# Kernel tuning notes

Measured on AMD Instinct MI355X. Metric: run time of the kernel, lower is better.

## Reference

```python
import jax, jax.numpy as jnp
import numpy as np

B, S, HID = 2, 2048, 2048
H, HKV = 16, 4
D = HID // H          # 128
N_REP = H // HKV      # 4
ROPE_THETA = 1000000.0


def _rope_tables(seq_len, head_dim, theta):
    inv_freq = 1.0 / (theta ** (jnp.arange(0, head_dim, 2, dtype=jnp.float32) / head_dim))
    freqs = jnp.arange(seq_len, dtype=jnp.float32)[:, None] * inv_freq[None, :]  # [S, D/2]
    emb = jnp.concatenate([freqs, freqs], axis=-1)  # [S, D]
    return jnp.cos(emb), jnp.sin(emb)


def setup_inputs() -> dict:
    key = jax.random.key(0)
    ks = jax.random.split(key, 6)
    cos, sin = _rope_tables(S, D, ROPE_THETA)
    sc = 0.02
    return {
        "x": jax.random.normal(ks[0], (B, S, HID), jnp.float32),
        "cos": cos,
        "sin": sin,
        "Wq": jax.random.normal(ks[1], (HID, H * D), jnp.float32) * sc,
        "Wk": jax.random.normal(ks[2], (HID, HKV * D), jnp.float32) * sc,
        "Wv": jax.random.normal(ks[3], (HID, HKV * D), jnp.float32) * sc,
        "Wo": jax.random.normal(ks[4], (H * D, HID), jnp.float32) * sc,
    }


def _rotate_half(t):
    t1, t2 = jnp.split(t, 2, axis=-1)
    return jnp.concatenate([-t2, t1], axis=-1)


def reference(x, cos, sin, Wq, Wk, Wv, Wo):
    b, s, _ = x.shape
    q = (x @ Wq).reshape(b, s, H, D)    # [b,s,H,d]
    k = (x @ Wk).reshape(b, s, HKV, D)  # [b,s,Hkv,d]
    v = (x @ Wv).reshape(b, s, HKV, D)

    # RoPE (cos/sin broadcast over head axis)
    c = cos[:s, None, :]  # [s,1,d]
    sn = sin[:s, None, :]
    q = q * c + _rotate_half(q) * sn
    k = k * c + _rotate_half(k) * sn

    # GQA: repeat kv heads (interleaved, matching repeat_kv)
    k = jnp.repeat(k, N_REP, axis=2)  # [b,s,H,d]
    v = jnp.repeat(v, N_REP, axis=2)

    q = q.transpose(0, 2, 1, 3)  # [b,H,s,d]
    k = k.transpose(0, 2, 1, 3)
    v = v.transpose(0, 2, 1, 3)

    scale = 1.0 / jnp.sqrt(jnp.asarray(D, x.dtype))
    scores = jnp.einsum("bhqd,bhkd->bhqk", q, k) * scale
    causal = jnp.tril(jnp.ones((s, s), dtype=bool))
    scores = jnp.where(causal[None, None], scores, jnp.asarray(-jnp.inf, scores.dtype))
    probs = jax.nn.softmax(scores, axis=-1)
    out = jnp.einsum("bhqk,bhkd->bhqd", probs, v)
    out = out.transpose(0, 2, 1, 3).reshape(b, s, H * D)
    return out @ Wo
```

## Files before the change

kernel.cpp:

```cpp
#include <hip/hip_runtime.h>
#include <cstdint>

#define B_    2
#define S_    2048
#define HID_  2048
#define H_    16
#define HKV_  4
#define D_    128
#define SCALE_ 0.08838834764831845f
#define LOG2E_ 1.4426950408889634f
#define K1_   (SCALE_ * LOG2E_)
#define THRS_ 62.75f

typedef __bf16 bf16x8 __attribute__((ext_vector_type(8)));
typedef float  f32x4  __attribute__((ext_vector_type(4)));
using u16 = unsigned short;

static __device__ __forceinline__ u16 f2bf(float f) {
  union { float f; uint32_t u; } c; c.f = f;
  uint32_t u = c.u;
  return (u16)((u + 0x7FFFu + ((u >> 16) & 1u)) >> 16);
}
static __device__ __forceinline__ float bf2f(u16 h) {
  union { uint32_t u; float f; } c; c.u = ((uint32_t)h) << 16;
  return c.f;
}
static __device__ __forceinline__ void async16(const u16* g, u16* lds) {
  __builtin_amdgcn_global_load_lds((const __attribute__((address_space(1))) void*)g,
                                   (__attribute__((address_space(3))) void*)lds, 16, 0, 0);
}

__global__ __launch_bounds__(256) void prep_cast_weights(const float* __restrict__ x,
                                                         const float* __restrict__ Wq,
                                                         const float* __restrict__ Wk,
                                                         const float* __restrict__ Wv,
                                                         const float* __restrict__ Wo,
                                                         u16* __restrict__ xb,
                                                         u16* __restrict__ Wt,
                                                         u16* __restrict__ Wot) {
  __shared__ float tile[32][33];
  const int t = blockIdx.x;
  const int tid = threadIdx.x;
  if (t < 8192) {
    const int i = t * 256 + tid;
    float4 v = ((const float4*)x)[i];
    ushort4 o;
    o.x = f2bf(v.x); o.y = f2bf(v.y); o.z = f2bf(v.z); o.w = f2bf(v.w);
    ((ushort4*)xb)[i] = o;
    return;
  }
  const int tw = t - 8192;
  const float* W; u16* Dst; int N, lt;
  if (tw < 4096)      { W = Wq; Dst = Wt;                        N = 2048; lt = tw; }
  else if (tw < 5120) { W = Wk; Dst = Wt + (size_t)2048 * 2048;  N = 512;  lt = tw - 4096; }
  else if (tw < 6144) { W = Wv; Dst = Wt + (size_t)2560 * 2048;  N = 512;  lt = tw - 5120; }
  else                { W = Wo; Dst = Wot;                       N = 2048; lt = tw - 6144; }
  const int tx = tid & 31, ty = tid >> 5;
  const int tn = N >> 5;
  const int n0 = (lt % tn) * 32, k0 = (lt / tn) * 32;
#pragma unroll
  for (int j = 0; j < 32; j += 8)
    tile[ty + j][tx] = W[(size_t)(k0 + ty + j) * N + n0 + tx];
  __syncthreads();
#pragma unroll
  for (int j = 0; j < 32; j += 8)
    Dst[(size_t)(n0 + ty + j) * 2048 + k0 + tx] = f2bf(tile[tx][ty + j]);
}

__global__ __launch_bounds__(256) void prep_rope_vt(const u16* __restrict__ qkv,
                                                    const float* __restrict__ cosb,
                                                    const float* __restrict__ sinb,
                                                    u16* __restrict__ Qr, u16* __restrict__ Kr,
                                                    u16* __restrict__ Vt) {
  __shared__ u16 tile[32][34];
  const int NQ2 = B_ * S_ * H_ * 32;
  const int NK2 = B_ * S_ * HKV_ * 32;
  const int blk = blockIdx.x;
  const int tid = threadIdx.x;
  if (blk < 10240) {
    const int idx = blk * 256 + tid;
    if (idx < NQ2) {
      const int j = (idx & 31) * 2, rest = idx >> 5;
      const int h = rest & 15, srow = rest >> 4;
      const int s = srow & (S_ - 1);
      const u16* base = qkv + (size_t)srow * 3072 + h * 128;
      const float2 cc = *(const float2*)&cosb[s * 128 + j];
      const float2 ss = *(const float2*)&sinb[s * 128 + j];
      const ushort2 av = *(const ushort2*)&base[j];
      const ushort2 bv = *(const ushort2*)&base[j + 64];
      const float a0 = bf2f(av.x), a1 = bf2f(av.y);
      const float b0 = bf2f(bv.x), b1 = bf2f(bv.y);
      const size_t qo = (((size_t)(srow >> 11) * H_ + h) * S_ + s) * D_;
      ushort2 lo, hi;
      lo.x = f2bf(a0 * cc.x - b0 * ss.x); lo.y = f2bf(a1 * cc.y - b1 * ss.y);
      hi.x = f2bf(b0 * cc.x + a0 * ss.x); hi.y = f2bf(b1 * cc.y + a1 * ss.y);
      *(ushort2*)&Qr[qo + j]      = lo;
      *(ushort2*)&Qr[qo + j + 64] = hi;
    } else if (idx < NQ2 + NK2) {
      const int t2 = idx - NQ2;
      const int j = (t2 & 31) * 2, rest = t2 >> 5;
      const int kv = rest & 3, srow = rest >> 2;
      const int s = srow & (S_ - 1);
      const u16* base = qkv + (size_t)srow * 3072 + 2048 + kv * 128;
      const float2 cc = *(const float2*)&cosb[s * 128 + j];
      const float2 ss = *(const float2*)&sinb[s * 128 + j];
      const ushort2 av = *(const ushort2*)&base[j];
      const ushort2 bv = *(const ushort2*)&base[j + 64];
      const float a0 = bf2f(av.x), a1 = bf2f(av.y);
      const float b0 = bf2f(bv.x), b1 = bf2f(bv.y);
      const size_t ko = (((size_t)(srow >> 11) * HKV_ + kv) * S_ + s) * D_;
      ushort2 lo, hi;
      lo.x = f2bf(a0 * cc.x - b0 * ss.x); lo.y = f2bf(a1 * cc.y - b1 * ss.y);
      hi.x = f2bf(b0 * cc.x + a0 * ss.x); hi.y = f2bf(b1 * cc.y + a1 * ss.y);
      *(ushort2*)&Kr[ko + j]      = lo;
      *(ushort2*)&Kr[ko + j + 64] = hi;
    }
    return;
  }
  const int lt = blk - 10240;
  const int bx = lt & 3, by = (lt >> 2) & 63, mat = lt >> 8;
  const int b = mat >> 2, kv = mat & 3;
  const int d0 = bx * 32, s0 = by * 32;
  const int tx = tid & 31, ty = tid >> 5;
#pragma unroll
  for (int j = 0; j < 32; j += 8)
    tile[ty + j][tx] = qkv[(size_t)(b * S_ + s0 + ty + j) * 3072 + 2560 + kv * 128 + d0 + tx];
  __syncthreads();
  const int sc  = s0 + tx;
  const int t64 = sc & 63;
  const int p   = ((t64 >> 5) * 4 + ((t64 >> 2) & 3)) * 8 + ((t64 >> 4) & 1) * 4 + (t64 & 3);
  const int scp = (sc & ~63) | p;
#pragma unroll
  for (int j = 0; j < 32; j += 8)
    Vt[((size_t)mat * D_ + d0 + ty + j) * S_ + scp] = tile[tx][ty + j];
}

template<int BF16OUT>
__global__ __launch_bounds__(256, 4) void gemm_bt(const u16* __restrict__ A,
                                                  const u16* __restrict__ Bt,
                                                  void* __restrict__ Cv,
                                                  int M, int N, int K, int gx) {
  const int nwg = (int)gridDim.x;
  const int bid = (int)blockIdx.x;
  const int qq = nwg >> 3, rr = nwg & 7;
  const int xcd = bid & 7, pos = bid >> 3;
  const int wg = ((xcd < rr) ? xcd * (qq + 1) : rr * (qq + 1) + (xcd - rr) * qq) + pos;
  const int bm = (wg % gx) * 128;
  const int bn = (wg / gx) * 128;

  __shared__ __align__(16) u16 Ash[128 * 64];
  __shared__ __align__(16) u16 Bsh[128 * 64];
  const int tid = threadIdx.x;
  const int w = tid >> 6, l = tid & 63;
  const int wm = (w >> 1) * 64, wn = (w & 1) * 64;

  const f32x4 z4 = {0.f, 0.f, 0.f, 0.f};
  f32x4 acc[4][4];
#pragma unroll
  for (int i = 0; i < 4; ++i)
#pragma unroll
    for (int j = 0; j < 4; ++j) acc[i][j] = z4;

  const int srow = w * 8 + (l >> 3);
  const int schunk = l & 7;

  for (int k0 = 0; k0 < K; k0 += 64) {
#pragma unroll
    for (int i = 0; i < 4; ++i) {
      const int row = i * 32 + srow;
      const int ch = schunk ^ (row & 7);
      async16(A + (size_t)(bm + row) * K + k0 + ch * 8, &Ash[(i * 4 + w) * 512]);
      async16(Bt + (size_t)(bn + row) * K + k0 + ch * 8, &Bsh[(i * 4 + w) * 512]);
    }
    asm volatile("s_waitcnt vmcnt(0)" ::: "memory");
    __syncthreads();
#pragma unroll
    for (int kc = 0; kc < 2; ++kc) {
      bf16x8 af[4], bfr[4];
#pragma unroll
      for (int mi = 0; mi < 4; ++mi) {
        const int r = wm + mi * 16 + (l & 15);
        const int c2 = (kc * 4 + (l >> 4)) ^ (r & 7);
        af[mi] = *(const bf16x8*)&Ash[r * 64 + c2 * 8];
      }
#pragma unroll
      for (int ni = 0; ni < 4; ++ni) {
        const int r = wn + ni * 16 + (l & 15);
        const int c2 = (kc * 4 + (l >> 4)) ^ (r & 7);
        bfr[ni] = *(const bf16x8*)&Bsh[r * 64 + c2 * 8];
      }
#pragma unroll
      for (int mi = 0; mi < 4; ++mi)
#pragma unroll
        for (int ni = 0; ni < 4; ++ni)
          acc[mi][ni] = __builtin_amdgcn_mfma_f32_16x16x32_bf16(af[mi], bfr[ni], acc[mi][ni], 0, 0, 0);
    }
    __syncthreads();
  }
#pragma unroll
  for (int mi = 0; mi < 4; ++mi) {
    const int r0 = bm + wm + mi * 16 + ((l >> 4) << 2);
#pragma unroll
    for (int ni = 0; ni < 4; ++ni) {
      const int c = bn + wn + ni * 16 + (l & 15);
#pragma unroll
      for (int j = 0; j < 4; ++j) {
        if (BF16OUT) ((u16*)Cv)[(size_t)(r0 + j) * N + c] = f2bf(acc[mi][ni][j]);
        else         ((float*)Cv)[(size_t)(r0 + j) * N + c] = acc[mi][ni][j];
      }
    }
  }
}

__global__ __launch_bounds__(256, 3) void attn_kernel(const u16* __restrict__ Q,
                                                      const u16* __restrict__ Kc,
                                                      const u16* __restrict__ Vt,
                                                      u16* __restrict__ O) {
  const int bid = blockIdx.x;
  const int p   = bid & 7;
  const int hs  = (bid >> 3) & 3;
  const int qt  = 31 - (bid >> 5);
  const int b   = p >> 2;
  const int kvh = p & 3;
  const int h   = kvh * 4 + hs;
  const int bh  = b * 16 + h;
  const int tid = threadIdx.x;
  const int w = tid >> 6, l = tid & 63;
  const int g = l >> 4, c = l & 15;
  const int q0 = qt * 64;

  __shared__ __align__(16) u16 Ksh[64 * 128];
  __shared__ __align__(16) u16 VshF[2 * 128 * 64];

  const u16* Kbase = Kc + ((size_t)(b * HKV_ + kvh) * S_) * D_;
  const u16* Vbase = Vt + ((size_t)(b * HKV_ + kvh) * D_) * S_;

  bf16x8 qf[4];
  {
    const u16* qp = Q + ((size_t)bh * S_ + q0 + w * 16 + c) * D_ + g * 8;
#pragma unroll
    for (int kc = 0; kc < 4; ++kc) qf[kc] = *(const bf16x8*)(qp + kc * 32);
  }

  int srcK[4], srcV[4];
#pragma unroll
  for (int i = 0; i < 4; ++i) {
    const int rK = i * 16 + w * 4 + g;
    srcK[i] = rK * 128 + (c ^ (rK & 7)) * 8;
    const int dV = i * 32 + w * 8 + (l >> 3);
    srcV[i] = dV * S_ + ((l & 7) ^ (dV & 7)) * 8;
  }

  const f32x4 z4 = {0.f, 0.f, 0.f, 0.f};
  f32x4 oacc[8];
#pragma unroll
  for (int nb = 0; nb < 8; ++nb) oacc[nb] = z4;
  float m_i = -1e30f, l_i = 0.f;

  auto stageK = [&](int kv0) {
#pragma unroll
    for (int i = 0; i < 4; ++i)
      async16(Kbase + (size_t)kv0 * 128 + srcK[i], &Ksh[i * 2048 + w * 512]);
  };
  auto stageV = [&](int buf, int kv0) {
#pragma unroll
    for (int i = 0; i < 4; ++i)
      async16(Vbase + kv0 + srcV[i], &VshF[buf * 8192 + i * 2048 + w * 512]);
  };

  const int nt = qt + 1;
  stageV(0, 0);
  stageK(0);

  for (int t = 0; t < nt; ++t) {
    const int cur = t & 1;
    asm volatile("s_waitcnt vmcnt(0)" ::: "memory");
    __syncthreads();
    if (t + 1 < nt) stageV(cur ^ 1, (t + 1) << 6);

    f32x4 sf[4];
#pragma unroll
    for (int nb = 0; nb < 4; ++nb) sf[nb] = z4;

    __builtin_amdgcn_s_setprio(1);
#pragma unroll
    for (int kc = 0; kc < 4; ++kc) {
#pragma unroll
      for (int nb = 0; nb < 4; ++nb) {
        const int r = nb * 16 + c;
        const int s2 = (kc * 4 + g) ^ (c & 7);
        const bf16x8 kf = *(const bf16x8*)&Ksh[r * 128 + s2 * 8];
        sf[nb] = __builtin_amdgcn_mfma_f32_16x16x32_bf16(kf, qf[kc], sf[nb], 0, 0, 0);
      }
    }
    __builtin_amdgcn_s_setprio(0);

    __syncthreads();
    if (t + 1 < nt) stageK((t + 1) << 6);

    {
      const int kv0 = t << 6;
      const int qcol = q0 + w * 16 + c;
      const bool doMask = (t == nt - 1);
      float mx = -3e38f;
#pragma unroll
      for (int nb = 0; nb < 4; ++nb)
#pragma unroll
        for (int jj = 0; jj < 4; ++jj) {
          float sv = sf[nb][jj];
          if (doMask) {
            const int kk = kv0 + nb * 16 + g * 4 + jj;
            sv = (kk > qcol) ? -3e38f : sv;
            sf[nb][jj] = sv;
          }
          mx = fmaxf(mx, sv);
        }
      mx = fmaxf(mx, __shfl_xor(mx, 16));
      mx = fmaxf(mx, __shfl_xor(mx, 32));

      if (__all(mx <= m_i + THRS_)) {
        const float mk = m_i * K1_;
        float rs = 0.f;
#pragma unroll
        for (int nb = 0; nb < 4; ++nb)
#pragma unroll
          for (int jj = 0; jj < 4; ++jj) {
            const float p2 = exp2f(fmaf(sf[nb][jj], K1_, -mk));
            sf[nb][jj] = p2;
            rs += p2;
          }
        rs += __shfl_xor(rs, 16);
        rs += __shfl_xor(rs, 32);
        l_i += rs;
      } else {
        const float mnew = fmaxf(m_i, mx);
        const float fsc = exp2f((m_i - mnew) * K1_);
        m_i = mnew;
        const float mk = mnew * K1_;
        float rs = 0.f;
#pragma unroll
        for (int nb = 0; nb < 4; ++nb)
#pragma unroll
          for (int jj = 0; jj < 4; ++jj) {
            const float p2 = exp2f(fmaf(sf[nb][jj], K1_, -mk));
            sf[nb][jj] = p2;
            rs += p2;
          }
        rs += __shfl_xor(rs, 16);
        rs += __shfl_xor(rs, 32);
        l_i = l_i * fsc + rs;
        float fq[4];
#pragma unroll
        for (int j = 0; j < 4; ++j) fq[j] = __shfl(fsc, g * 4 + j);
#pragma unroll
        for (int nb = 0; nb < 8; ++nb)
#pragma unroll
          for (int j = 0; j < 4; ++j) oacc[nb][j] *= fq[j];
      }
    }

    bf16x8 pa, pb;
#pragma unroll
    for (int jj = 0; jj < 4; ++jj) {
      pa[jj] = (__bf16)sf[0][jj]; pa[4 + jj] = (__bf16)sf[1][jj];
      pb[jj] = (__bf16)sf[2][jj]; pb[4 + jj] = (__bf16)sf[3][jj];
    }

    const char* Vb = (const char*)&VshF[cur * 8192] + c * 128;
    __builtin_amdgcn_s_setprio(1);
#pragma unroll
    for (int kc2 = 0; kc2 < 2; ++kc2) {
      const bf16x8 pfr = kc2 ? pb : pa;
      const int s2v = ((kc2 * 4 + g) ^ (c & 7)) << 4;
#pragma unroll
      for (int nb = 0; nb < 8; ++nb) {
        const bf16x8 vf = *(const bf16x8*)(Vb + nb * 2048 + s2v);
        oacc[nb] = __builtin_amdgcn_mfma_f32_16x16x32_bf16(pfr, vf, oacc[nb], 0, 0, 0);
      }
    }
    __builtin_amdgcn_s_setprio(0);
  }

#pragma unroll
  for (int j = 0; j < 4; ++j) {
    const float li = __shfl(l_i, g * 4 + j);
    const float inv = 1.f / li;
    const int srow = q0 + w * 16 + g * 4 + j;
    u16* op = O + ((size_t)(b * S_ + srow)) * HID_ + h * D_ + c;
#pragma unroll
    for (int nb = 0; nb < 8; ++nb) op[nb * 16] = f2bf(oacc[nb][j] * inv);
  }
}

extern "C" void kernel_launch(void* const* d_in, const int* in_sizes, int n_in,
                              void* d_out, int out_size, void* d_ws, size_t ws_size,
                              hipStream_t stream) {
  const float* x    = (const float*)d_in[0];
  const float* cosb = (const float*)d_in[1];
  const float* sinb = (const float*)d_in[2];
  const float* Wq   = (const float*)d_in[3];
  const float* Wk   = (const float*)d_in[4];
  const float* Wv   = (const float*)d_in[5];
  const float* Wo   = (const float*)d_in[6];
  float* out = (float*)d_out;

  u16*   xb   = (u16*)d_ws;
  u16*   Wt   = xb  + (size_t)4096 * 2048;
  u16*   Wot  = Wt  + (size_t)3072 * 2048;
  u16*   qkv  = Wot + (size_t)2048 * 2048;
  u16*   Qr   = qkv + (size_t)4096 * 3072;
  u16*   Kr   = Qr  + (size_t)B_ * H_ * S_ * D_;
  u16*   Vtb  = Kr  + (size_t)B_ * HKV_ * S_ * D_;
  u16*   Ob   = Vtb + (size_t)B_ * HKV_ * S_ * D_;

  prep_cast_weights<<<dim3(18432), 256, 0, stream>>>(x, Wq, Wk, Wv, Wo, xb, Wt, Wot);

  gemm_bt<1><<<dim3(768), 256, 0, stream>>>(xb, Wt, qkv, 4096, 3072, 2048, 32);

  prep_rope_vt<<<dim3(12288), 256, 0, stream>>>(qkv, cosb, sinb, Qr, Kr, Vtb);

  attn_kernel<<<dim3(1024), 256, 0, stream>>>(Qr, Kr, Vtb, Ob);

  gemm_bt<0><<<dim3(512), 256, 0, stream>>>(Ob, Wot, out, 4096, 2048, 2048, 32);
}
```

Measured before the change: 198.6 us.

## Widen attention query tile to 128 rows with double-buffered K/V

Each attention block now covers 128 query rows, with two 16-row groups per wave, instead of 64, so every K/V tile loaded into shared memory feeds twice as many MFMAs. K is now double-buffered together with V, which removes the second barrier in each iteration. Waves skip KV tiles that lie entirely above their causal rows. The block-to-tile order changes so heavy and light query tiles are interleaved, and the launch bounds drop to 2 blocks per CU to allow more registers. In exchange the grid is halved to 512 blocks, which lowers occupancy and parallelism, and waves in a block become unevenly loaded on the diagonal tiles.

```diff
diff --git a/kernel.cpp b/kernel.cpp
--- a/kernel.cpp
+++ b/kernel.cpp
@@ -212,14 +212,14 @@
   }
 }
 
-__global__ __launch_bounds__(256, 3) void attn_kernel(const u16* __restrict__ Q,
+__global__ __launch_bounds__(256, 2) void attn_kernel(const u16* __restrict__ Q,
                                                       const u16* __restrict__ Kc,
                                                       const u16* __restrict__ Vt,
                                                       u16* __restrict__ O) {
   const int bid = blockIdx.x;
   const int p   = bid & 7;
   const int hs  = (bid >> 3) & 3;
-  const int qt  = 31 - (bid >> 5);
+  const int qt  = (bid < 256) ? (15 - (bid >> 5)) : ((bid >> 5) - 8);
   const int b   = p >> 2;
   const int kvh = p & 3;
   const int h   = kvh * 4 + hs;
@@ -227,19 +227,20 @@
   const int tid = threadIdx.x;
   const int w = tid >> 6, l = tid & 63;
   const int g = l >> 4, c = l & 15;
-  const int q0 = qt * 64;
-
-  __shared__ __align__(16) u16 Ksh[64 * 128];
+  const int q0 = qt * 128;
+
+  __shared__ __align__(16) u16 KshF[2 * 64 * 128];
   __shared__ __align__(16) u16 VshF[2 * 128 * 64];
 
   const u16* Kbase = Kc + ((size_t)(b * HKV_ + kvh) * S_) * D_;
   const u16* Vbase = Vt + ((size_t)(b * HKV_ + kvh) * D_) * S_;
 
-  bf16x8 qf[4];
-  {
-    const u16* qp = Q + ((size_t)bh * S_ + q0 + w * 16 + c) * D_ + g * 8;
-#pragma unroll
-    for (int kc = 0; kc < 4; ++kc) qf[kc] = *(const bf16x8*)(qp + kc * 32);
+  bf16x8 qf[2][4];
+#pragma unroll
+  for (int qg = 0; qg < 2; ++qg) {
+    const u16* qp = Q + ((size_t)bh * S_ + q0 + w * 32 + qg * 16 + c) * D_ + g * 8;
+#pragma unroll
+    for (int kc = 0; kc < 4; ++kc) qf[qg][kc] = *(const bf16x8*)(qp + kc * 32);
   }
 
   int srcK[4], srcV[4];
@@ -252,144 +253,153 @@
   }
 
   const f32x4 z4 = {0.f, 0.f, 0.f, 0.f};
-  f32x4 oacc[8];
-#pragma unroll
-  for (int nb = 0; nb < 8; ++nb) oacc[nb] = z4;
-  float m_i = -1e30f, l_i = 0.f;
-
-  auto stageK = [&](int kv0) {
-#pragma unroll
-    for (int i = 0; i < 4; ++i)
-      async16(Kbase + (size_t)kv0 * 128 + srcK[i], &Ksh[i * 2048 + w * 512]);
+  f32x4 oacc[2][8];
+#pragma unroll
+  for (int qg = 0; qg < 2; ++qg)
+#pragma unroll
+    for (int nb = 0; nb < 8; ++nb) oacc[qg][nb] = z4;
+  float m_i[2] = {-1e30f, -1e30f}, l_i[2] = {0.f, 0.f};
+
+  auto stage = [&](int buf, int kv0) {
+#pragma unroll
+    for (int i = 0; i < 4; ++i) {
+      async16(Kbase + (size_t)kv0 * 128 + srcK[i], &KshF[buf * 8192 + i * 2048 + w * 512]);
+      async16(Vbase + kv0 + srcV[i],               &VshF[buf * 8192 + i * 2048 + w * 512]);
+    }
   };
-  auto stageV = [&](int buf, int kv0) {
-#pragma unroll
-    for (int i = 0; i < 4; ++i)
-      async16(Vbase + kv0 + srcV[i], &VshF[buf * 8192 + i * 2048 + w * 512]);
-  };
-
-  const int nt = qt + 1;
-  stageV(0, 0);
-  stageK(0);
+
+  const int nt = 2 * (qt + 1);
+  stage(0, 0);
 
   for (int t = 0; t < nt; ++t) {
     const int cur = t & 1;
+    const int kv0 = t << 6;
     asm volatile("s_waitcnt vmcnt(0)" ::: "memory");
     __syncthreads();
-    if (t + 1 < nt) stageV(cur ^ 1, (t + 1) << 6);
-
-    f32x4 sf[4];
-#pragma unroll
-    for (int nb = 0; nb < 4; ++nb) sf[nb] = z4;
-
-    __builtin_amdgcn_s_setprio(1);
-#pragma unroll
-    for (int kc = 0; kc < 4; ++kc) {
-#pragma unroll
-      for (int nb = 0; nb < 4; ++nb) {
-        const int r = nb * 16 + c;
-        const int s2 = (kc * 4 + g) ^ (c & 7);
-        const bf16x8 kf = *(const bf16x8*)&Ksh[r * 128 + s2 * 8];
-        sf[nb] = __builtin_amdgcn_mfma_f32_16x16x32_bf16(kf, qf[kc], sf[nb], 0, 0, 0);
-      }
-    }
-    __builtin_amdgcn_s_setprio(0);
-
-    __syncthreads();
-    if (t + 1 < nt) stageK((t + 1) << 6);
-
-    {
-      const int kv0 = t << 6;
-      const int qcol = q0 + w * 16 + c;
-      const bool doMask = (t == nt - 1);
-      float mx = -3e38f;
-#pragma unroll
-      for (int nb = 0; nb < 4; ++nb)
-#pragma unroll
-        for (int jj = 0; jj < 4; ++jj) {
-          float sv = sf[nb][jj];
-          if (doMask) {
-            const int kk = kv0 + nb * 16 + g * 4 + jj;
-            sv = (kk > qcol) ? -3e38f : sv;
-            sf[nb][jj] = sv;
+    if (t + 1 < nt) stage(cur ^ 1, (t + 1) << 6);
+
+    if (kv0 <= q0 + w * 32 + 31) {
+      const u16* Kb = &KshF[cur * 8192];
+
+      f32x4 sf[2][4];
+#pragma unroll
+      for (int qg = 0; qg < 2; ++qg)
+#pragma unroll
+        for (int nb = 0; nb < 4; ++nb) sf[qg][nb] = z4;
+
+      __builtin_amdgcn_s_setprio(1);
+#pragma unroll
+      for (int kc = 0; kc < 4; ++kc) {
+#pragma unroll
+        for (int nb = 0; nb < 4; ++nb) {
+          const int r = nb * 16 + c;
+          const int s2 = (kc * 4 + g) ^ (c & 7);
+          const bf16x8 kf = *(const bf16x8*)&Kb[r * 128 + s2 * 8];
+          sf[0][nb] = __builtin_amdgcn_mfma_f32_16x16x32_bf16(kf, qf[0][kc], sf[0][nb], 0, 0, 0);
+          sf[1][nb] = __builtin_amdgcn_mfma_f32_16x16x32_bf16(kf, qf[1][kc], sf[1][nb], 0, 0, 0);
+        }
+      }
+      __builtin_amdgcn_s_setprio(0);
+
+#pragma unroll
+      for (int qg = 0; qg < 2; ++qg) {
+        const int qcol = q0 + w * 32 + qg * 16 + c;
+        const bool doMask = (kv0 + 63 > q0 + w * 32 + qg * 16);
+        float mx = -3e38f;
+#pragma unroll
+        for (int nb = 0; nb < 4; ++nb)
+#pragma unroll
+          for (int jj = 0; jj < 4; ++jj) {
+            float sv = sf[qg][nb][jj];
+            if (doMask) {
+              const int kk = kv0 + nb * 16 + g * 4 + jj;
+              sv = (kk > qcol) ? -3e38f : sv;
+              sf[qg][nb][jj] = sv;
+            }
+            mx = fmaxf(mx, sv);
           }
-          mx = fmaxf(mx, sv);
+        mx = fmaxf(mx, __shfl_xor(mx, 16));
+        mx = fmaxf(mx, __shfl_xor(mx, 32));
+
+        if (__all(mx <= m_i[qg] + THRS_)) {
+          const float mk = m_i[qg] * K1_;
+          float rs = 0.f;
+#pragma unroll
+          for (int nb = 0; nb < 4; ++nb)
+#pragma unroll
+            for (int jj = 0; jj < 4; ++jj) {
+              const float p2 = exp2f(fmaf(sf[qg][nb][jj], K1_, -mk));
+              sf[qg][nb][jj] = p2;
+              rs += p2;
+            }
+          rs += __shfl_xor(rs, 16);
+          rs += __shfl_xor(rs, 32);
+          l_i[qg] += rs;
+        } else {
+          const float mnew = fmaxf(m_i[qg], mx);
+          const float fsc = exp2f((m_i[qg] - mnew) * K1_);
+          m_i[qg] = mnew;
+          const float mk = mnew * K1_;
+          float rs = 0.f;
+#pragma unroll
+          for (int nb = 0; nb < 4; ++nb)
+#pragma unroll
+            for (int jj = 0; jj < 4; ++jj) {
+              const float p2 = exp2f(fmaf(sf[qg][nb][jj], K1_, -mk));
+              sf[qg][nb][jj] = p2;
+              rs += p2;
+            }
+          rs += __shfl_xor(rs, 16);
+          rs += __shfl_xor(rs, 32);
+          l_i[qg] = l_i[qg] * fsc + rs;
+          float fq[4];
+#pragma unroll
+          for (int j = 0; j < 4; ++j) fq[j] = __shfl(fsc, g * 4 + j);
+#pragma unroll
+          for (int nb = 0; nb < 8; ++nb)
+#pragma unroll
+            for (int j = 0; j < 4; ++j) oacc[qg][nb][j] *= fq[j];
         }
-      mx = fmaxf(mx, __shfl_xor(mx, 16));
-      mx = fmaxf(mx, __shfl_xor(mx, 32));
-
-      if (__all(mx <= m_i + THRS_)) {
-        const float mk = m_i * K1_;
-        float rs = 0.f;
-#pragma unroll
-        for (int nb = 0; nb < 4; ++nb)
-#pragma unroll
-          for (int jj = 0; jj < 4; ++jj) {
-            const float p2 = exp2f(fmaf(sf[nb][jj], K1_, -mk));
-            sf[nb][jj] = p2;
-            rs += p2;
-          }
-        rs += __shfl_xor(rs, 16);
-        rs += __shfl_xor(rs, 32);
-        l_i += rs;
-      } else {
-        const float mnew = fmaxf(m_i, mx);
-        const float fsc = exp2f((m_i - mnew) * K1_);
-        m_i = mnew;
-        const float mk = mnew * K1_;
-        float rs = 0.f;
-#pragma unroll
-        for (int nb = 0; nb < 4; ++nb)
-#pragma unroll
-          for (int jj = 0; jj < 4; ++jj) {
-            const float p2 = exp2f(fmaf(sf[nb][jj], K1_, -mk));
-            sf[nb][jj] = p2;
-            rs += p2;
-          }
-        rs += __shfl_xor(rs, 16);
-        rs += __shfl_xor(rs, 32);
-        l_i = l_i * fsc + rs;
-        float fq[4];
-#pragma unroll
-        for (int j = 0; j < 4; ++j) fq[j] = __shfl(fsc, g * 4 + j);
-#pragma unroll
-        for (int nb = 0; nb < 8; ++nb)
-#pragma unroll
-          for (int j = 0; j < 4; ++j) oacc[nb][j] *= fq[j];
-      }
-    }
-
-    bf16x8 pa, pb;
-#pragma unroll
-    for (int jj = 0; jj < 4; ++jj) {
-      pa[jj] = (__bf16)sf[0][jj]; pa[4 + jj] = (__bf16)sf[1][jj];
-      pb[jj] = (__bf16)sf[2][jj]; pb[4 + jj] = (__bf16)sf[3][jj];
-    }
-
-    const char* Vb = (const char*)&VshF[cur * 8192] + c * 128;
-    __builtin_amdgcn_s_setprio(1);
-#pragma unroll
-    for (int kc2 = 0; kc2 < 2; ++kc2) {
-      const bf16x8 pfr = kc2 ? pb : pa;
-      const int s2v = ((kc2 * 4 + g) ^ (c & 7)) << 4;
-#pragma unroll
-      for (int nb = 0; nb < 8; ++nb) {
-        const bf16x8 vf = *(const bf16x8*)(Vb + nb * 2048 + s2v);
-        oacc[nb] = __builtin_amdgcn_mfma_f32_16x16x32_bf16(pfr, vf, oacc[nb], 0, 0, 0);
-      }
-    }
-    __builtin_amdgcn_s_setprio(0);
-  }
-
-#pragma unroll
-  for (int j = 0; j < 4; ++j) {
-    const float li = __shfl(l_i, g * 4 + j);
-    const float inv = 1.f / li;
-    const int srow = q0 + w * 16 + g * 4 + j;
-    u16* op = O + ((size_t)(b * S_ + srow)) * HID_ + h * D_ + c;
-#pragma unroll
-    for (int nb = 0; nb < 8; ++nb) op[nb * 16] = f2bf(oacc[nb][j] * inv);
-  }
+      }
+
+      bf16x8 paq0, paq1, pbq0, pbq1;
+#pragma unroll
+      for (int jj = 0; jj < 4; ++jj) {
+        paq0[jj] = (__bf16)sf[0][0][jj]; paq0[4 + jj] = (__bf16)sf[0][1][jj];
+        pbq0[jj] = (__bf16)sf[0][2][jj]; pbq0[4 + jj] = (__bf16)sf[0][3][jj];
+        paq1[jj] = (__bf16)sf[1][0][jj]; paq1[4 + jj] = (__bf16)sf[1][1][jj];
+        pbq1[jj] = (__bf16)sf[1][2][jj]; pbq1[4 + jj] = (__bf16)sf[1][3][jj];
+      }
+
+      const char* Vb = (const char*)&VshF[cur * 8192] + c * 128;
+      __builtin_amdgcn_s_setprio(1);
+#pragma unroll
+      for (int kc2 = 0; kc2 < 2; ++kc2) {
+        const bf16x8 pa0 = kc2 ? pbq0 : paq0;
+        const bf16x8 pa1 = kc2 ? pbq1 : paq1;
+        const int s2v = ((kc2 * 4 + g) ^ (c & 7)) << 4;
+#pragma unroll
+        for (int nb = 0; nb < 8; ++nb) {
+          const bf16x8 vf = *(const bf16x8*)(Vb + nb * 2048 + s2v);
+          oacc[0][nb] = __builtin_amdgcn_mfma_f32_16x16x32_bf16(pa0, vf, oacc[0][nb], 0, 0, 0);
+          oacc[1][nb] = __builtin_amdgcn_mfma_f32_16x16x32_bf16(pa1, vf, oacc[1][nb], 0, 0, 0);
+        }
+      }
+      __builtin_amdgcn_s_setprio(0);
+    }
+  }
+
+#pragma unroll
+  for (int qg = 0; qg < 2; ++qg)
+#pragma unroll
+    for (int j = 0; j < 4; ++j) {
+      const float li = __shfl(l_i[qg], g * 4 + j);
+      const float inv = 1.f / li;
+      const int srow = q0 + w * 32 + qg * 16 + g * 4 + j;
+      u16* op = O + ((size_t)(b * S_ + srow)) * HID_ + h * D_ + c;
+#pragma unroll
+      for (int nb = 0; nb < 8; ++nb) op[nb * 16] = f2bf(oacc[qg][nb][j] * inv);
+    }
 }
 
 extern "C" void kernel_launch(void* const* d_in, const int* in_sizes, int n_in,
@@ -419,7 +429,7 @@
 
   prep_rope_vt<<<dim3(12288), 256, 0, stream>>>(qkv, cosb, sinb, Qr, Kr, Vtb);
 
-  attn_kernel<<<dim3(1024), 256, 0, stream>>>(Qr, Kr, Vtb, Ob);
+  attn_kernel<<<dim3(512), 256, 0, stream>>>(Qr, Kr, Vtb, Ob);
 
   gemm_bt<0><<<dim3(512), 256, 0, stream>>>(Ob, Wot, out, 4096, 2048, 2048, 32);
 }
```

Result: slower. 220.8 us (+11.2%).
